# Kernel optimization log

Hardware: AMD Instinct MI355X
Metric: run time of the kernel (lower is better)

Reference implementation:

```python
import jax, jax.numpy as jnp
import numpy as np

N = 65536      # total nodes (BS graphs of 4096 nodes)
E = 524288     # edges
BS = 16
EPS = 1e-5
D_ATT = 8      # attention d_model
H_ATT = 4      # attention heads
SQRT_D = np.float32(np.sqrt(8.0))


def gcn_conv(x, src, dst, W, b):
    # PyG GCNConv: add self-loops, sym-normalized sum aggregation of x @ W
    n = x.shape[0]
    h = x @ W  # [N, out]
    loop = jnp.arange(n, dtype=src.dtype)
    s = jnp.concatenate([src, loop])
    d = jnp.concatenate([dst, loop])
    deg = jax.ops.segment_sum(jnp.ones_like(d, x.dtype), d, num_segments=n)
    dinv = jax.lax.rsqrt(jnp.maximum(deg, 1.0))  # deg >= 1 due to self loops
    norm = dinv[s] * dinv[d]                      # [E+N]
    out = jax.ops.segment_sum(h[s] * norm[:, None], d, num_segments=n)
    return out + b


def sage_conv(x, src, dst, Wl, Wr, b):
    # PyG SAGEConv (mean aggr): lin_l(mean_{j in N(i)} x_j) + lin_r(x_i)
    n = x.shape[0]
    agg = jax.ops.segment_sum(x[src], dst, num_segments=n)
    cnt = jax.ops.segment_sum(jnp.ones_like(dst, x.dtype), dst, num_segments=n)
    mean = agg / jnp.maximum(cnt, 1.0)[:, None]
    return mean @ Wl + x @ Wr + b


def batch_norm(x):
    # F.batch_norm(x, None, None, training=True): per-feature, no affine, biased var
    mu = x.mean(axis=0)
    var = x.var(axis=0)
    return (x - mu) * jax.lax.rsqrt(var + EPS)


def attention_plug(plug, Wq, bq, Wk, bk, Wv, bv, Wfc, bfc):
    q = (plug @ Wq + bq).reshape(BS, 1, H_ATT, D_ATT)
    k = (plug @ Wk + bk).reshape(BS, 1, H_ATT, D_ATT)
    v = (plug @ Wv + bv).reshape(BS, 1, H_ATT, D_ATT)
    scores = jnp.einsum('bihd,bijd->bihj', q, k) / SQRT_D  # [BS,1,H,H]
    logits = scores[:, 0]                                   # squeeze -> [BS,H,H]
    u = jax.random.uniform(jax.random.key(42), logits.shape, minval=1e-9, maxval=1.0)
    gumbel = -jnp.log(-jnp.log(u))
    attn = jax.nn.softmax(logits + gumbel, axis=-1) * SQRT_D  # gumbel_softmax(tau=1)
    attn = attn.reshape(BS, 1, H_ATT, H_ATT)
    out = jnp.einsum('bihj,bijd->bihd', attn, v)  # [BS,1,H,D]
    out = out.reshape(BS, D_ATT, H_ATT).reshape(BS, D_ATT * H_ATT)  # view then flatten
    return out @ Wfc + bfc  # [BS, 4]


def setup_inputs():
    key = jax.random.key(0)
    ks = jax.random.split(key, 24)
    w = lambda k, shp, fan: (jax.random.normal(k, shp, jnp.float32) / np.sqrt(fan)).astype(jnp.float32)
    inp = {}
    inp['x'] = jax.random.normal(ks[0], (N, 640), jnp.float32)
    inp['edge_index'] = jax.random.randint(ks[1], (2, E), 0, N, jnp.int32)
    inp['gender'] = jax.random.uniform(ks[2], (BS, 2), jnp.float32)
    inp['age'] = jax.random.uniform(ks[3], (BS, 1), jnp.float32)
    inp['handed'] = jax.random.uniform(ks[4], (BS, 5), jnp.float32)
    inp['W1'] = w(ks[5], (640, 320), 640); inp['b1'] = jnp.zeros((320,), jnp.float32)
    inp['Wl2'] = w(ks[6], (320, 180), 320); inp['Wr2'] = w(ks[7], (320, 180), 320); inp['b2'] = jnp.zeros((180,), jnp.float32)
    inp['Wl3'] = w(ks[8], (180, 90), 180); inp['Wr3'] = w(ks[9], (180, 90), 180); inp['b3'] = jnp.zeros((90,), jnp.float32)
    inp['Wl4'] = w(ks[10], (90, 50), 90); inp['Wr4'] = w(ks[11], (90, 50), 90); inp['b4'] = jnp.zeros((50,), jnp.float32)
    inp['Wq'] = w(ks[12], (8, 32), 8); inp['bq'] = jnp.zeros((32,), jnp.float32)
    inp['Wk'] = w(ks[13], (8, 32), 8); inp['bk'] = jnp.zeros((32,), jnp.float32)
    inp['Wv'] = w(ks[14], (8, 32), 8); inp['bv'] = jnp.zeros((32,), jnp.float32)
    inp['Wfc'] = w(ks[15], (32, 4), 32); inp['bfc'] = jnp.zeros((4,), jnp.float32)
    inp['Wf1'] = w(ks[16], (54, 32), 54); inp['bf1'] = jnp.zeros((32,), jnp.float32)
    inp['Wf2'] = w(ks[17], (32, 16), 32); inp['bf2'] = jnp.zeros((16,), jnp.float32)
    inp['Wf3'] = w(ks[18], (16, 1), 16); inp['bf3'] = jnp.zeros((1,), jnp.float32)
    return inp


def reference(x, edge_index, gender, age, handed,
              W1, b1, Wl2, Wr2, b2, Wl3, Wr3, b3, Wl4, Wr4, b4,
              Wq, bq, Wk, bk, Wv, bv, Wfc, bfc,
              Wf1, bf1, Wf2, bf2, Wf3, bf3):
    src, dst = edge_index[0], edge_index[1]
    h = batch_norm(jax.nn.leaky_relu(gcn_conv(x, src, dst, W1, b1)))
    h = batch_norm(jax.nn.leaky_relu(sage_conv(h, src, dst, Wl2, Wr2, b2)))
    h = batch_norm(jax.nn.leaky_relu(sage_conv(h, src, dst, Wl3, Wr3, b3)))
    h = batch_norm(jax.nn.leaky_relu(sage_conv(h, src, dst, Wl4, Wr4, b4)))
    batch = jnp.arange(N) // (N // BS)
    pooled = jax.ops.segment_sum(h, batch, num_segments=BS)  # global_add_pool [BS,50]
    plug = jnp.concatenate([gender, age, handed], axis=1)    # [BS,8]
    plugx = attention_plug(plug, Wq, bq, Wk, bk, Wv, bv, Wfc, bfc)  # [BS,4]
    emb = jnp.concatenate([pooled, plugx], axis=1)           # [BS,54]
    out = ((emb @ Wf1 + bf1) @ Wf2 + bf2) @ Wf3 + bf3        # [BS,1]
    return out, emb
```

## Files before the change

### kernel.cpp

```cpp
#include <hip/hip_runtime.h>
#include <cstdint>

#define NN 65536
#define EE 524288
#define BS_ 16

typedef unsigned short u16;
typedef unsigned int u32;
typedef __attribute__((ext_vector_type(8))) short short8v;
typedef __attribute__((ext_vector_type(4))) float f32x4;

__device__ __forceinline__ u16 f2bf(float f) {
    u32 u = __float_as_uint(f);
    u32 r = (u + 0x7fffu + ((u >> 16) & 1u)) >> 16;
    return (u16)r;
}
__device__ __forceinline__ float bff(u16 h) {
    return __uint_as_float(((u32)h) << 16);
}

__device__ __forceinline__ float bnleaky(float v, float s, float q) {
    const float invN = 1.0f / 65536.0f;
    float mu = s * invN;
    float var = q * invN - mu * mu;
    float u = v >= 0.f ? v : 0.01f * v;
    return (u - mu) * rsqrtf(var + 1e-5f);
}

__device__ __forceinline__ u32 rotl32(u32 x, int d) {
    return (x << d) | (x >> (32 - d));
}
__device__ __forceinline__ void threefry_0_42(u32& x0, u32& x1) {
    const u32 ks0 = 0u, ks1 = 42u, ks2 = 0u ^ 42u ^ 0x1BD11BDAu;
    x0 += ks0; x1 += ks1;
#define RND(r) { x0 += x1; x1 = rotl32(x1, r); x1 ^= x0; }
    RND(13) RND(15) RND(26) RND(6)  x0 += ks1; x1 += ks2 + 1u;
    RND(17) RND(29) RND(16) RND(24) x0 += ks2; x1 += ks0 + 2u;
    RND(13) RND(15) RND(26) RND(6)  x0 += ks0; x1 += ks1 + 3u;
    RND(17) RND(29) RND(16) RND(24) x0 += ks1; x1 += ks2 + 4u;
    RND(13) RND(15) RND(26) RND(6)  x0 += ks2; x1 += ks0 + 5u;
#undef RND
}

__global__ void k_indeg(const int* __restrict__ dst, int* __restrict__ indeg) {
    int e = blockIdx.x * 256 + threadIdx.x;
    if (e < EE) atomicAdd(&indeg[dst[e]], 1);
}

__global__ void k_scan(const int* __restrict__ indeg, int* __restrict__ rowptr,
                       int* __restrict__ cursor) {
    __shared__ int psum[256];
    int t = threadIdx.x;
    int base = t * 256;
    int s = 0;
    for (int i = 0; i < 256; ++i) s += indeg[base + i];
    psum[t] = s;
    __syncthreads();
    for (int off = 1; off < 256; off <<= 1) {
        int v = (t >= off) ? psum[t - off] : 0;
        __syncthreads();
        psum[t] += v;
        __syncthreads();
    }
    int run = (t == 0) ? 0 : psum[t - 1];
    for (int i = 0; i < 256; ++i) {
        rowptr[base + i] = run;
        cursor[base + i] = run;
        run += indeg[base + i];
    }
    if (t == 255) rowptr[NN] = run;
}

__global__ void k_fill(const int* __restrict__ src, const int* __restrict__ dst,
                       int* __restrict__ cursor, int* __restrict__ csr) {
    int e = blockIdx.x * 256 + threadIdx.x;
    if (e < EE) {
        int d = dst[e];
        int p = atomicAdd(&cursor[d], 1);
        csr[p] = src[e];
    }
}

__global__ void k_dinv(const int* __restrict__ indeg, float* __restrict__ dinv) {
    int i = blockIdx.x * 256 + threadIdx.x;
    if (i < NN) dinv[i] = rsqrtf((float)indeg[i] + 1.0f);
}

__global__ void k_wsplit2(const float* __restrict__ Wr, const float* __restrict__ Wlsrc,
                          int K, int N, int KP, int CS, int NPW,
                          u16* __restrict__ Wh, u16* __restrict__ Wl) {
    int idx = blockIdx.x * 256 + threadIdx.x;
    if (idx >= NPW * KP) return;
    int n = idx / KP, k = idx % KP;
    float v = 0.f;
    if (n < CS) {
        if (n < N && k < K) v = Wr[(size_t)k * N + n];
    } else {
        int n2 = n - CS;
        if (Wlsrc != nullptr && n2 < N && k < K) v = Wlsrc[(size_t)k * N + n2];
    }
    u16 h = f2bf(v);
    u16 l = f2bf(v - bff(h));
    Wh[idx] = h;
    Wl[idx] = l;
}

template <bool HASB, bool HASBN>
__global__ __launch_bounds__(256, 3) void k_gemm_mfma(
    const float* __restrict__ A, const u16* __restrict__ Wgh, const u16* __restrict__ Wgl,
    int KP, int lda, const float* __restrict__ bns,
    const float* __restrict__ bias, float* __restrict__ O1, float* __restrict__ O2,
    int N, int CS) {
    __shared__ u16 Ah[64][72];
    __shared__ u16 Wh[128][72];
    __shared__ u16 Wl[128][72];

    const int t = threadIdx.x;
    const int bm = blockIdx.x * 64;
    const int bn = blockIdx.y * 128;
    const int lane = t & 63;
    const int wid = t >> 6;
    const int wr = wid >> 1, wc = wid & 1;

    f32x4 acc[2][4];
#pragma unroll
    for (int m = 0; m < 2; ++m)
#pragma unroll
        for (int n = 0; n < 4; ++n) acc[m][n] = (f32x4){0.f, 0.f, 0.f, 0.f};

    const int sr = t >> 4;
    const int sc4 = (t & 15) * 4;

    for (int k0 = 0; k0 < KP; k0 += 64) {
        float4 s4, q4;
        if (HASBN) {
            s4 = *(const float4*)(bns + k0 + sc4);
            q4 = *(const float4*)(bns + 512 + k0 + sc4);
        }
#pragma unroll
        for (int p = 0; p < 4; ++p) {
            int rr = sr + 16 * p;
            float4 v = *(const float4*)(A + (size_t)(bm + rr) * lda + k0 + sc4);
            if (HASBN) {
                v.x = bnleaky(v.x, s4.x, q4.x);
                v.y = bnleaky(v.y, s4.y, q4.y);
                v.z = bnleaky(v.z, s4.z, q4.z);
                v.w = bnleaky(v.w, s4.w, q4.w);
            }
            uint2 hh;
            hh.x = (u32)f2bf(v.x) | ((u32)f2bf(v.y) << 16);
            hh.y = (u32)f2bf(v.z) | ((u32)f2bf(v.w) << 16);
            *(uint2*)&Ah[rr][sc4] = hh;
        }
#pragma unroll
        for (int p = 0; p < 8; ++p) {
            int nn = sr + 16 * p;
            size_t go = (size_t)(bn + nn) * KP + k0 + sc4;
            *(uint2*)&Wh[nn][sc4] = *(const uint2*)(Wgh + go);
            *(uint2*)&Wl[nn][sc4] = *(const uint2*)(Wgl + go);
        }
        __syncthreads();
        const int fr = lane & 15;
        const int kg = (lane >> 4) * 8;
#pragma unroll
        for (int kk = 0; kk < 64; kk += 32) {
            short8v a_h[2], w_h[4], w_l[4];
#pragma unroll
            for (int m = 0; m < 2; ++m)
                a_h[m] = *(const short8v*)&Ah[wr * 32 + m * 16 + fr][kk + kg];
#pragma unroll
            for (int n = 0; n < 4; ++n) {
                w_h[n] = *(const short8v*)&Wh[wc * 64 + n * 16 + fr][kk + kg];
                w_l[n] = *(const short8v*)&Wl[wc * 64 + n * 16 + fr][kk + kg];
            }
#pragma unroll
            for (int m = 0; m < 2; ++m)
#pragma unroll
                for (int n = 0; n < 4; ++n) {
                    acc[m][n] = __builtin_amdgcn_mfma_f32_16x16x32_bf16(a_h[m], w_h[n], acc[m][n], 0, 0, 0);
                    acc[m][n] = __builtin_amdgcn_mfma_f32_16x16x32_bf16(a_h[m], w_l[n], acc[m][n], 0, 0, 0);
                }
        }
        __syncthreads();
    }
    const int fr = lane & 15, fq = lane >> 4;
#pragma unroll
    for (int m = 0; m < 2; ++m) {
        int row = bm + wr * 32 + m * 16 + fq * 4;
#pragma unroll
        for (int n = 0; n < 4; ++n) {
            int col = bn + wc * 64 + n * 16 + fr;
            if (col < CS) {
                float b = (HASB && col < N) ? bias[col] : 0.f;
#pragma unroll
                for (int e = 0; e < 4; ++e)
                    O1[(size_t)(row + e) * CS + col] = acc[m][n][e] + b;
            } else if (O2 != nullptr) {
                int c2 = col - CS;
#pragma unroll
                for (int e = 0; e < 4; ++e)
                    O2[(size_t)(row + e) * CS + c2] = acc[m][n][e];
            }
        }
    }
}

__global__ __launch_bounds__(256) void k_gcn_agg320(const float* __restrict__ h,
                                                    const int* __restrict__ rowptr,
                                                    const int* __restrict__ csr,
                                                    const float* __restrict__ dinv,
                                                    const float* __restrict__ bias,
                                                    float* __restrict__ out) {
    int lane = threadIdx.x & 63;
    int n = blockIdx.x * 4 + (threadIdx.x >> 6);
    bool has1 = lane < 16;
    float di = dinv[n];
    float s2 = di * di;
    const float4* hn = (const float4*)(h + (size_t)n * 320);
    float4 v0 = hn[lane];
    float4 a0 = make_float4(v0.x * s2, v0.y * s2, v0.z * s2, v0.w * s2);
    float4 a1 = make_float4(0.f, 0.f, 0.f, 0.f);
    if (has1) {
        float4 v1 = hn[64 + lane];
        a1 = make_float4(v1.x * s2, v1.y * s2, v1.z * s2, v1.w * s2);
    }
    int e = rowptr[n], e1 = rowptr[n + 1];
    for (; e + 4 <= e1; e += 4) {
        int s0 = csr[e], s1 = csr[e + 1], s2i = csr[e + 2], s3 = csr[e + 3];
        float w0 = dinv[s0] * di, w1 = dinv[s1] * di, w2 = dinv[s2i] * di, w3 = dinv[s3] * di;
        const float4* p0 = (const float4*)(h + (size_t)s0 * 320);
        const float4* p1 = (const float4*)(h + (size_t)s1 * 320);
        const float4* p2 = (const float4*)(h + (size_t)s2i * 320);
        const float4* p3 = (const float4*)(h + (size_t)s3 * 320);
        float4 u0 = p0[lane], u1 = p1[lane], u2 = p2[lane], u3 = p3[lane];
        a0.x += u0.x * w0 + u1.x * w1 + u2.x * w2 + u3.x * w3;
        a0.y += u0.y * w0 + u1.y * w1 + u2.y * w2 + u3.y * w3;
        a0.z += u0.z * w0 + u1.z * w1 + u2.z * w2 + u3.z * w3;
        a0.w += u0.w * w0 + u1.w * w1 + u2.w * w2 + u3.w * w3;
        if (has1) {
            float4 x0 = p0[64 + lane], x1 = p1[64 + lane], x2 = p2[64 + lane], x3 = p3[64 + lane];
            a1.x += x0.x * w0 + x1.x * w1 + x2.x * w2 + x3.x * w3;
            a1.y += x0.y * w0 + x1.y * w1 + x2.y * w2 + x3.y * w3;
            a1.z += x0.z * w0 + x1.z * w1 + x2.z * w2 + x3.z * w3;
            a1.w += x0.w * w0 + x1.w * w1 + x2.w * w2 + x3.w * w3;
        }
    }
    for (; e < e1; ++e) {
        int s = csr[e];
        float w = dinv[s] * di;
        const float4* hs = (const float4*)(h + (size_t)s * 320);
        float4 u0 = hs[lane];
        a0.x = fmaf(u0.x, w, a0.x); a0.y = fmaf(u0.y, w, a0.y);
        a0.z = fmaf(u0.z, w, a0.z); a0.w = fmaf(u0.w, w, a0.w);
        if (has1) {
            float4 u1 = hs[64 + lane];
            a1.x = fmaf(u1.x, w, a1.x); a1.y = fmaf(u1.y, w, a1.y);
            a1.z = fmaf(u1.z, w, a1.z); a1.w = fmaf(u1.w, w, a1.w);
        }
    }
    const float4* b4 = (const float4*)bias;
    float4* on = (float4*)(out + (size_t)n * 320);
    float4 bb = b4[lane];
    on[lane] = make_float4(a0.x + bb.x, a0.y + bb.y, a0.z + bb.z, a0.w + bb.w);
    if (has1) {
        float4 bb1 = b4[64 + lane];
        on[64 + lane] = make_float4(a1.x + bb1.x, a1.y + bb1.y, a1.z + bb1.z, a1.w + bb1.w);
    }
}

template <int CH, int LOG_NPW>
__global__ __launch_bounds__(256) void k_agg_add(const float* __restrict__ T,
                                                 const int* __restrict__ rowptr,
                                                 const int* __restrict__ csr,
                                                 const int* __restrict__ indeg,
                                                 float* __restrict__ C) {
    constexpr int NPW = 1 << LOG_NPW;
    constexpr int LPN = 64 >> LOG_NPW;
    constexpr int SC = CH * 4;
    int lane = threadIdx.x & 63;
    int sub = lane / LPN;
    int ch = lane & (LPN - 1);
    int n = (blockIdx.x * 4 + (threadIdx.x >> 6)) * NPW + sub;
    bool act = ch < CH;
    float4 acc = make_float4(0.f, 0.f, 0.f, 0.f);
    int e = rowptr[n], e1 = rowptr[n + 1];
    for (; e + 4 <= e1; e += 4) {
        int s0 = csr[e], s1 = csr[e + 1], s2 = csr[e + 2], s3 = csr[e + 3];
        if (act) {
            float4 u0 = *(const float4*)(T + (size_t)s0 * SC + ch * 4);
            float4 u1 = *(const float4*)(T + (size_t)s1 * SC + ch * 4);
            float4 u2 = *(const float4*)(T + (size_t)s2 * SC + ch * 4);
            float4 u3 = *(const float4*)(T + (size_t)s3 * SC + ch * 4);
            acc.x += (u0.x + u1.x) + (u2.x + u3.x);
            acc.y += (u0.y + u1.y) + (u2.y + u3.y);
            acc.z += (u0.z + u1.z) + (u2.z + u3.z);
            acc.w += (u0.w + u1.w) + (u2.w + u3.w);
        }
    }
    for (; e < e1; ++e) {
        int s = csr[e];
        if (act) {
            float4 u = *(const float4*)(T + (size_t)s * SC + ch * 4);
            acc.x += u.x; acc.y += u.y; acc.z += u.z; acc.w += u.w;
        }
    }
    int cnt = indeg[n];
    float inv = 1.0f / (float)(cnt > 1 ? cnt : 1);
    if (act) {
        float4* cp = (float4*)(C + (size_t)n * SC + ch * 4);
        float4 c = *cp;
        c.x = fmaf(acc.x, inv, c.x);
        c.y = fmaf(acc.y, inv, c.y);
        c.z = fmaf(acc.z, inv, c.z);
        c.w = fmaf(acc.w, inv, c.w);
        *cp = c;
    }
}

template <int D, int STR>
__global__ __launch_bounds__(256) void k_bn_stats(const float* __restrict__ x,
                                                  float* __restrict__ stats) {
    constexpr int NC = (D + 255) / 256;
    int t = threadIdx.x;
    int r0 = blockIdx.x * 64;
    float s[NC], q[NC];
#pragma unroll
    for (int i = 0; i < NC; ++i) { s[i] = 0.f; q[i] = 0.f; }
#pragma unroll 4
    for (int r = r0; r < r0 + 64; ++r) {
        const float* row = x + (size_t)r * STR;
#pragma unroll
        for (int i = 0; i < NC; ++i) {
            int c = t + 256 * i;
            if (c < D) {
                float v = row[c];
                v = v >= 0.f ? v : 0.01f * v;
                s[i] += v;
                q[i] += v * v;
            }
        }
    }
#pragma unroll
    for (int i = 0; i < NC; ++i) {
        int c = t + 256 * i;
        if (c < D) {
            atomicAdd(&stats[c], s[i]);
            atomicAdd(&stats[512 + c], q[i]);
        }
    }
}

template <int STR>
__global__ __launch_bounds__(256) void k_bn_apply(float* __restrict__ x,
                                                  const float* __restrict__ stats) {
    size_t total4 = (size_t)NN * STR / 4;
    size_t stride = (size_t)gridDim.x * 256;
    for (size_t i = (size_t)blockIdx.x * 256 + threadIdx.x; i < total4; i += stride) {
        int c = (int)((i * 4) % STR);
        float4 v = ((const float4*)x)[i];
        float4 m4 = *(const float4*)(stats + c);
        float4 q4 = *(const float4*)(stats + 512 + c);
        float4 o;
        o.x = bnleaky(v.x, m4.x, q4.x);
        o.y = bnleaky(v.y, m4.y, q4.y);
        o.z = bnleaky(v.z, m4.z, q4.z);
        o.w = bnleaky(v.w, m4.w, q4.w);
        ((float4*)x)[i] = o;
    }
}

__global__ __launch_bounds__(256) void k_pool(const float* __restrict__ h,
                                              float* __restrict__ pooled) {
    int blk = blockIdx.x;
    int batch = blk >> 4, seg = blk & 15;
    int f = threadIdx.x & 63, g = threadIdx.x >> 6;
    size_t base = ((size_t)batch * 4096 + seg * 256 + g) * 64 + f;
    float acc = 0.f;
    for (int i = 0; i < 64; ++i) acc += h[base + (size_t)i * 256];
    atomicAdd(&pooled[batch * 64 + f], acc);
}

__global__ __launch_bounds__(256) void k_head(
    const float* __restrict__ gender, const float* __restrict__ age,
    const float* __restrict__ handed, const float* __restrict__ Wq,
    const float* __restrict__ bq, const float* __restrict__ Wk,
    const float* __restrict__ bk, const float* __restrict__ Wv,
    const float* __restrict__ bv, const float* __restrict__ Wfc,
    const float* __restrict__ bfc, const float* __restrict__ Wf1,
    const float* __restrict__ bf1, const float* __restrict__ Wf2,
    const float* __restrict__ bf2, const float* __restrict__ Wf3,
    const float* __restrict__ bf3, const float* __restrict__ pooled,
    float* __restrict__ dout) {
    __shared__ float plug[BS_][8];
    __shared__ float qs[BS_][32], ks[BS_][32], vs[BS_][32];
    __shared__ float gum[256];
    __shared__ float x32[BS_][32];
    __shared__ float px[BS_][4];
    __shared__ float embs[BS_][54];
    __shared__ float t1[BS_][32];
    __shared__ float t2[BS_][16];
    int t = threadIdx.x;

    if (t < 128) {
        int b = t >> 3, c = t & 7;
        float v;
        if (c < 2) v = gender[b * 2 + c];
        else if (c == 2) v = age[b];
        else v = handed[b * 5 + (c - 3)];
        plug[b][c] = v;
    }
    {
        u32 lane = (u32)(t & 127);
        u32 a = lane, b2 = lane + 128u;
        threefry_0_42(a, b2);
        u32 bits = (t < 128) ? a : b2;
        float u = __uint_as_float((bits >> 9) | 0x3f800000u) - 1.0f;
        const float mn = 1e-9f;
        u = u * (1.0f - mn) + mn;
        u = fmaxf(mn, u);
        gum[t] = -logf(-logf(u));
    }
    __syncthreads();
    for (int idx = t; idx < 512; idx += 256) {
        int b = idx >> 5, c = idx & 31;
        float aq = bq[c], ak = bk[c], av = bv[c];
#pragma unroll
        for (int i = 0; i < 8; ++i) {
            float p = plug[b][i];
            aq = fmaf(p, Wq[i * 32 + c], aq);
            ak = fmaf(p, Wk[i * 32 + c], ak);
            av = fmaf(p, Wv[i * 32 + c], av);
        }
        qs[b][c] = aq; ks[b][c] = ak; vs[b][c] = av;
    }
    __syncthreads();
    if (t < 64) {
        int b = t >> 2, h = t & 3;
        const float isq = 0.35355339059327373f;
        const float sq = 2.8284271247461903f;
        float sc[4];
#pragma unroll
        for (int j = 0; j < 4; ++j) {
            float d = 0.f;
#pragma unroll
            for (int dd = 0; dd < 8; ++dd) d = fmaf(qs[b][h * 8 + dd], ks[b][j * 8 + dd], d);
            sc[j] = d * isq + gum[b * 16 + h * 4 + j];
        }
        float m = fmaxf(fmaxf(sc[0], sc[1]), fmaxf(sc[2], sc[3]));
        float e0 = expf(sc[0] - m), e1 = expf(sc[1] - m), e2 = expf(sc[2] - m), e3 = expf(sc[3] - m);
        float sum = e0 + e1 + e2 + e3;
        float a0 = e0 / sum * sq, a1 = e1 / sum * sq, a2 = e2 / sum * sq, a3 = e3 / sum * sq;
#pragma unroll
        for (int dd = 0; dd < 8; ++dd) {
            float o = a0 * vs[b][0 * 8 + dd] + a1 * vs[b][1 * 8 + dd] +
                      a2 * vs[b][2 * 8 + dd] + a3 * vs[b][3 * 8 + dd];
            x32[b][h * 8 + dd] = o;
        }
    }
    __syncthreads();
    if (t < 64) {
        int b = t >> 2, n = t & 3;
        float a = bfc[n];
#pragma unroll
        for (int m = 0; m < 32; ++m) a = fmaf(x32[b][m], Wfc[m * 4 + n], a);
        px[b][n] = a;
    }
    __syncthreads();
    for (int idx = t; idx < BS_ * 54; idx += 256) {
        int b = idx / 54, c = idx % 54;
        float v = (c < 50) ? pooled[b * 64 + c] : px[b][c - 50];
        embs[b][c] = v;
        dout[16 + idx] = v;
    }
    __syncthreads();
    for (int idx = t; idx < 512; idx += 256) {
        int b = idx >> 5, c = idx & 31;
        float a = bf1[c];
#pragma unroll
        for (int k = 0; k < 54; ++k) a = fmaf(embs[b][k], Wf1[k * 32 + c], a);
        t1[b][c] = a;
    }
    __syncthreads();
    {
        int b = t >> 4, c = t & 15;
        float a = bf2[c];
#pragma unroll
        for (int k = 0; k < 32; ++k) a = fmaf(t1[b][k], Wf2[k * 16 + c], a);
        t2[b][c] = a;
    }
    __syncthreads();
    if (t < 16) {
        float a = bf3[0];
#pragma unroll
        for (int k = 0; k < 16; ++k) a = fmaf(t2[t][k], Wf3[k], a);
        dout[t] = a;
    }
}

extern "C" void kernel_launch(void* const* d_in, const int* in_sizes, int n_in,
                              void* d_out, int out_size, void* d_ws, size_t ws_size,
                              hipStream_t stream) {
    const float* x      = (const float*)d_in[0];
    const int*   ei     = (const int*)d_in[1];
    const float* gender = (const float*)d_in[2];
    const float* age    = (const float*)d_in[3];
    const float* handed = (const float*)d_in[4];
    const float* W1  = (const float*)d_in[5];
    const float* b1  = (const float*)d_in[6];
    const float* Wl2 = (const float*)d_in[7];
    const float* Wr2 = (const float*)d_in[8];
    const float* b2  = (const float*)d_in[9];
    const float* Wl3 = (const float*)d_in[10];
    const float* Wr3 = (const float*)d_in[11];
    const float* b3  = (const float*)d_in[12];
    const float* Wl4 = (const float*)d_in[13];
    const float* Wr4 = (const float*)d_in[14];
    const float* b4  = (const float*)d_in[15];
    const float* Wq  = (const float*)d_in[16];
    const float* bq  = (const float*)d_in[17];
    const float* Wk  = (const float*)d_in[18];
    const float* bk  = (const float*)d_in[19];
    const float* Wv  = (const float*)d_in[20];
    const float* bv  = (const float*)d_in[21];
    const float* Wfc = (const float*)d_in[22];
    const float* bfc = (const float*)d_in[23];
    const float* Wf1 = (const float*)d_in[24];
    const float* bf1 = (const float*)d_in[25];
    const float* Wf2 = (const float*)d_in[26];
    const float* bf2 = (const float*)d_in[27];
    const float* Wf3 = (const float*)d_in[28];
    const float* bf3 = (const float*)d_in[29];

    const int* srcp = ei;
    const int* dstp = ei + EE;

    char* wsb = (char*)d_ws;
    size_t off = 0;
    auto alloc = [&](size_t bytes) -> char* {
        char* p = wsb + off;
        off += (bytes + 255) & ~(size_t)255;
        return p;
    };
    float* P = (float*)alloc((size_t)NN * 320 * 4);
    float* Q = (float*)alloc((size_t)NN * 320 * 4);
    float* R = (float*)alloc((size_t)NN * 192 * 4);
    float* T = (float*)alloc((size_t)NN * 192 * 4);
    int* indeg  = (int*)alloc((size_t)NN * 4);
    int* rowptr = (int*)alloc((size_t)(NN + 1) * 4);
    int* cursor = (int*)alloc((size_t)(NN + 1) * 4);
    int* csr    = (int*)alloc((size_t)EE * 4);
    float* dinv = (float*)alloc((size_t)NN * 4);
    float* stats  = (float*)alloc(4096 * 4);
    float* pooled = (float*)alloc(16 * 64 * 4);
    u16* W1h = (u16*)alloc((size_t)384 * 640 * 2);
    u16* W1l = (u16*)alloc((size_t)384 * 640 * 2);
    u16* W2h = (u16*)alloc((size_t)384 * 320 * 2);
    u16* W2l = (u16*)alloc((size_t)384 * 320 * 2);
    u16* W3h = (u16*)alloc((size_t)256 * 192 * 2);
    u16* W3l = (u16*)alloc((size_t)256 * 192 * 2);
    u16* W4h = (u16*)alloc((size_t)128 * 128 * 2);
    u16* W4l = (u16*)alloc((size_t)128 * 128 * 2);
    float* dout = (float*)d_out;

    hipMemsetAsync(indeg, 0, (size_t)NN * 4, stream);
    hipMemsetAsync(stats, 0, 4096 * 4, stream);
    k_indeg<<<EE / 256, 256, 0, stream>>>(dstp, indeg);
    k_scan<<<1, 256, 0, stream>>>(indeg, rowptr, cursor);
    k_fill<<<EE / 256, 256, 0, stream>>>(srcp, dstp, cursor, csr);
    k_dinv<<<NN / 256, 256, 0, stream>>>(indeg, dinv);

    k_wsplit2<<<(384 * 640 + 255) / 256, 256, 0, stream>>>(W1, nullptr, 640, 320, 640, 320, 384, W1h, W1l);
    k_wsplit2<<<(384 * 320 + 255) / 256, 256, 0, stream>>>(Wr2, Wl2, 320, 180, 320, 192, 384, W2h, W2l);
    k_wsplit2<<<(256 * 192 + 255) / 256, 256, 0, stream>>>(Wr3, Wl3, 180, 90, 192, 128, 256, W3h, W3l);
    k_wsplit2<<<(128 * 128 + 255) / 256, 256, 0, stream>>>(Wr4, Wl4, 90, 50, 128, 64, 128, W4h, W4l);

    k_gemm_mfma<false, false><<<dim3(1024, 3), 256, 0, stream>>>(
        x, W1h, W1l, 640, 640, nullptr, nullptr, P, nullptr, 320, 320);
    k_gcn_agg320<<<NN / 4, 256, 0, stream>>>(P, rowptr, csr, dinv, b1, Q);
    k_bn_stats<320, 320><<<1024, 256, 0, stream>>>(Q, stats);

    k_gemm_mfma<true, true><<<dim3(1024, 3), 256, 0, stream>>>(
        Q, W2h, W2l, 320, 320, stats, b2, R, T, 180, 192);
    k_agg_add<48, 0><<<NN / 4, 256, 0, stream>>>(T, rowptr, csr, indeg, R);
    k_bn_stats<180, 192><<<1024, 256, 0, stream>>>(R, stats + 1024);

    k_gemm_mfma<true, true><<<dim3(1024, 2), 256, 0, stream>>>(
        R, W3h, W3l, 192, 192, stats + 1024, b3, P, T, 90, 128);
    k_agg_add<32, 1><<<NN / 8, 256, 0, stream>>>(T, rowptr, csr, indeg, P);
    k_bn_stats<90, 128><<<1024, 256, 0, stream>>>(P, stats + 2048);

    k_gemm_mfma<true, true><<<dim3(1024, 1), 256, 0, stream>>>(
        P, W4h, W4l, 128, 128, stats + 2048, b4, Q, T, 50, 64);
    k_agg_add<16, 2><<<NN / 16, 256, 0, stream>>>(T, rowptr, csr, indeg, Q);
    k_bn_stats<50, 64><<<1024, 256, 0, stream>>>(Q, stats + 3072);
    k_bn_apply<64><<<2048, 256, 0, stream>>>(Q, stats + 3072);

    hipMemsetAsync(pooled, 0, 16 * 64 * 4, stream);
    k_pool<<<256, 256, 0, stream>>>(Q, pooled);
    k_head<<<1, 256, 0, stream>>>(gender, age, handed, Wq, bq, Wk, bk, Wv, bv,
                                  Wfc, bfc, Wf1, bf1, Wf2, bf2, Wf3, bf3, pooled, dout);
}
```

Before: 1.050 ms.

## Parallelize CSR scan and stream pre-swizzled weight tiles via direct global-to-LDS loads

The single-block prefix scan over node in-degrees becomes a three-kernel parallel scan (block reduce, scan of block sums, per-block scan with offsets), removing a long serial single-workgroup kernel. Weight split kernels now write bf16 hi/lo weights in a tiled, XOR-swizzled layout, and the GEMM loads each 128x64 weight tile directly into LDS with global_load_lds 16-byte copies instead of going through registers. The swizzle is meant to avoid LDS bank conflicts on MFMA fragment reads. The risks are two extra kernel launches and a reliance on the exact tile layout matching the LDS indexing.

```diff
diff --git a/kernel.cpp b/kernel.cpp
--- a/kernel.cpp
+++ b/kernel.cpp
@@ -17,6 +17,12 @@
 }
 __device__ __forceinline__ float bff(u16 h) {
     return __uint_as_float(((u32)h) << 16);
+}
+
+__device__ __forceinline__ void gload_lds16(const void* g, void* l) {
+    __builtin_amdgcn_global_load_lds(
+        (const __attribute__((address_space(1))) void*)g,
+        (__attribute__((address_space(3))) void*)l, 16, 0, 0);
 }
 
 __device__ __forceinline__ float bnleaky(float v, float s, float q) {
@@ -47,28 +53,50 @@
     if (e < EE) atomicAdd(&indeg[dst[e]], 1);
 }
 
-__global__ void k_scan(const int* __restrict__ indeg, int* __restrict__ rowptr,
-                       int* __restrict__ cursor) {
-    __shared__ int psum[256];
+__global__ void k_scan1(const int* __restrict__ indeg, int* __restrict__ bsum) {
+    __shared__ int red[256];
     int t = threadIdx.x;
-    int base = t * 256;
-    int s = 0;
-    for (int i = 0; i < 256; ++i) s += indeg[base + i];
-    psum[t] = s;
-    __syncthreads();
-    for (int off = 1; off < 256; off <<= 1) {
-        int v = (t >= off) ? psum[t - off] : 0;
+    red[t] = indeg[blockIdx.x * 256 + t];
+    __syncthreads();
+    for (int o = 128; o > 0; o >>= 1) {
+        if (t < o) red[t] += red[t + o];
         __syncthreads();
-        psum[t] += v;
+    }
+    if (t == 0) bsum[blockIdx.x] = red[0];
+}
+
+__global__ void k_scan2(const int* __restrict__ bsum, int* __restrict__ boff) {
+    __shared__ int ps[256];
+    int t = threadIdx.x;
+    int orig = bsum[t];
+    ps[t] = orig;
+    __syncthreads();
+    for (int o = 1; o < 256; o <<= 1) {
+        int v = (t >= o) ? ps[t - o] : 0;
         __syncthreads();
-    }
-    int run = (t == 0) ? 0 : psum[t - 1];
-    for (int i = 0; i < 256; ++i) {
-        rowptr[base + i] = run;
-        cursor[base + i] = run;
-        run += indeg[base + i];
-    }
-    if (t == 255) rowptr[NN] = run;
+        ps[t] += v;
+        __syncthreads();
+    }
+    boff[t] = ps[t] - orig;
+}
+
+__global__ void k_scan3(const int* __restrict__ indeg, const int* __restrict__ boff,
+                        int* __restrict__ rowptr, int* __restrict__ cursor) {
+    __shared__ int ps[256];
+    int b = blockIdx.x, t = threadIdx.x;
+    int v = indeg[b * 256 + t];
+    ps[t] = v;
+    __syncthreads();
+    for (int o = 1; o < 256; o <<= 1) {
+        int u = (t >= o) ? ps[t - o] : 0;
+        __syncthreads();
+        ps[t] += u;
+        __syncthreads();
+    }
+    int ex = boff[b] + ps[t] - v;
+    rowptr[b * 256 + t] = ex;
+    cursor[b * 256 + t] = ex;
+    if (b == 255 && t == 255) rowptr[NN] = ex + v;
 }
 
 __global__ void k_fill(const int* __restrict__ src, const int* __restrict__ dst,
@@ -101,8 +129,11 @@
     }
     u16 h = f2bf(v);
     u16 l = f2bf(v - bff(h));
-    Wh[idx] = h;
-    Wl[idx] = l;
+    int nb = n >> 7, nn = n & 127, kb = k >> 6, kk = k & 63;
+    size_t o = ((size_t)nb * (KP >> 6) + kb) * 8192
+             + nn * 64 + (((kk >> 3) ^ (nn & 7)) << 3) + (kk & 7);
+    Wh[o] = h;
+    Wl[o] = l;
 }
 
 template <bool HASB, bool HASBN>
@@ -112,12 +143,11 @@
     const float* __restrict__ bias, float* __restrict__ O1, float* __restrict__ O2,
     int N, int CS) {
     __shared__ u16 Ah[64][72];
-    __shared__ u16 Wh[128][72];
-    __shared__ u16 Wl[128][72];
+    __shared__ u16 WhL[8192];
+    __shared__ u16 WlL[8192];
 
     const int t = threadIdx.x;
     const int bm = blockIdx.x * 64;
-    const int bn = blockIdx.y * 128;
     const int lane = t & 63;
     const int wid = t >> 6;
     const int wr = wid >> 1, wc = wid & 1;
@@ -130,8 +160,19 @@
 
     const int sr = t >> 4;
     const int sc4 = (t & 15) * 4;
+    const int nkb = KP >> 6;
 
     for (int k0 = 0; k0 < KP; k0 += 64) {
+        {
+            const size_t wtile = ((size_t)blockIdx.y * nkb + (k0 >> 6)) * 8192;
+            const int cb = wid * 2048;
+#pragma unroll
+            for (int c = 0; c < 4; ++c) {
+                int o = cb + c * 512;
+                gload_lds16(Wgh + wtile + o + lane * 8, &WhL[o]);
+                gload_lds16(Wgl + wtile + o + lane * 8, &WlL[o]);
+            }
+        }
         float4 s4, q4;
         if (HASBN) {
             s4 = *(const float4*)(bns + k0 + sc4);
@@ -152,16 +193,10 @@
             hh.y = (u32)f2bf(v.z) | ((u32)f2bf(v.w) << 16);
             *(uint2*)&Ah[rr][sc4] = hh;
         }
-#pragma unroll
-        for (int p = 0; p < 8; ++p) {
-            int nn = sr + 16 * p;
-            size_t go = (size_t)(bn + nn) * KP + k0 + sc4;
-            *(uint2*)&Wh[nn][sc4] = *(const uint2*)(Wgh + go);
-            *(uint2*)&Wl[nn][sc4] = *(const uint2*)(Wgl + go);
-        }
         __syncthreads();
         const int fr = lane & 15;
-        const int kg = (lane >> 4) * 8;
+        const int kg8 = lane >> 4;
+        const int kg = kg8 * 8;
 #pragma unroll
         for (int kk = 0; kk < 64; kk += 32) {
             short8v a_h[2], w_h[4], w_l[4];
@@ -170,8 +205,11 @@
                 a_h[m] = *(const short8v*)&Ah[wr * 32 + m * 16 + fr][kk + kg];
 #pragma unroll
             for (int n = 0; n < 4; ++n) {
-                w_h[n] = *(const short8v*)&Wh[wc * 64 + n * 16 + fr][kk + kg];
-                w_l[n] = *(const short8v*)&Wl[wc * 64 + n * 16 + fr][kk + kg];
+                int r = wc * 64 + n * 16 + fr;
+                int slot = (kk >> 3) + kg8;
+                int o = r * 64 + ((slot ^ (r & 7)) << 3);
+                w_h[n] = *(const short8v*)&WhL[o];
+                w_l[n] = *(const short8v*)&WlL[o];
             }
 #pragma unroll
             for (int m = 0; m < 2; ++m)
@@ -183,6 +221,7 @@
         }
         __syncthreads();
     }
+    const int bn = blockIdx.y * 128;
     const int fr = lane & 15, fq = lane >> 4;
 #pragma unroll
     for (int m = 0; m < 2; ++m) {
@@ -550,6 +589,8 @@
     int* cursor = (int*)alloc((size_t)(NN + 1) * 4);
     int* csr    = (int*)alloc((size_t)EE * 4);
     float* dinv = (float*)alloc((size_t)NN * 4);
+    int* bsum   = (int*)alloc(256 * 4);
+    int* boff   = (int*)alloc(257 * 4);
     float* stats  = (float*)alloc(4096 * 4);
     float* pooled = (float*)alloc(16 * 64 * 4);
     u16* W1h = (u16*)alloc((size_t)384 * 640 * 2);
@@ -565,7 +606,9 @@
     hipMemsetAsync(indeg, 0, (size_t)NN * 4, stream);
     hipMemsetAsync(stats, 0, 4096 * 4, stream);
     k_indeg<<<EE / 256, 256, 0, stream>>>(dstp, indeg);
-    k_scan<<<1, 256, 0, stream>>>(indeg, rowptr, cursor);
+    k_scan1<<<256, 256, 0, stream>>>(indeg, bsum);
+    k_scan2<<<1, 256, 0, stream>>>(bsum, boff);
+    k_scan3<<<256, 256, 0, stream>>>(indeg, boff, rowptr, cursor);
     k_fill<<<EE / 256, 256, 0, stream>>>(srcp, dstp, cursor, csr);
     k_dinv<<<NN / 256, 256, 0, stream>>>(indeg, dinv);
 
```

After: 997.2 us. 5.1% less time.
